# Optimization experiments

Hardware: AMD Instinct MI355X
Metric: run time of the kernel (lower is better)

The kernel has to match this reference:

```python
import jax, jax.numpy as jnp
import numpy as np

N = 100000
E = 3200000
F_IN = 256
F_OUT = 256
HID = 64


def setup_inputs() -> dict:
    key = jax.random.key(0)
    ks = jax.random.split(key, 16)
    stdv = 1.0 / np.sqrt(F_OUT)
    std_att = 1.0 / np.sqrt(HID)
    std_att_vec = 1.0 / np.sqrt(3.0)
    u = lambda k, shape, s: jax.random.uniform(k, shape, jnp.float32, -s, s)
    return {
        "inputx": jax.random.normal(ks[0], (N, F_IN), jnp.float32),
        "row_A": jax.random.randint(ks[1], (E,), 0, N),
        "col_A": jax.random.randint(ks[2], (E,), 0, N),
        "val_A": jax.random.uniform(ks[3], (E,), jnp.float32),
        "row_A2": jax.random.randint(ks[4], (E,), 0, N),
        "col_A2": jax.random.randint(ks[5], (E,), 0, N),
        "val_A2": jax.random.uniform(ks[6], (E,), jnp.float32),
        "weight_A": u(ks[7], (F_IN, F_OUT), stdv),
        "weight_A2": u(ks[8], (F_IN, F_OUT), stdv),
        "weight_mlp": u(ks[9], (F_IN, F_OUT), stdv),
        "W_k0": u(ks[10], (F_OUT, HID), std_att),
        "W_k1": u(ks[11], (F_OUT, HID), std_att),
        "W_k2": u(ks[12], (F_OUT, HID), std_att),
        "att_vec_A": u(ks[13], (F_OUT, HID), std_att),
        "att_vec_A2": u(ks[14], (F_OUT, HID), std_att),
        "att_vec_mlp": u(ks[15], (F_OUT, HID), std_att),
        "att_vec": u(jax.random.fold_in(key, 99), (3, 3), std_att_vec),
    }


def _spmm(row, col, val, x, n):
    # COO sparse-dense matmul: out[r] += val_e * x[c]
    return jax.ops.segment_sum(val[:, None] * x[col], row, num_segments=n)


def reference(inputx, row_A, col_A, val_A, row_A2, col_A2, val_A2,
              weight_A, weight_A2, weight_mlp, W_k0, W_k1, W_k2,
              att_vec_A, att_vec_A2, att_vec_mlp, att_vec):
    n = inputx.shape[0]
    out_A = jax.nn.relu(_spmm(row_A, col_A, val_A, inputx @ weight_A, n))
    out_A2 = jax.nn.relu(_spmm(row_A2, col_A2, val_A2, inputx @ weight_A2, n))
    out_mlp = jax.nn.relu(inputx @ weight_mlp)
    # attention gating
    T = 3.0
    k0 = jnp.mean(out_A @ W_k0, axis=0, keepdims=True)    # [1, HID]
    k1 = jnp.mean(out_A2 @ W_k1, axis=0, keepdims=True)
    k2 = jnp.mean(out_mlp @ W_k2, axis=0, keepdims=True)
    logits = jnp.concatenate([
        (out_A @ att_vec_A) @ k0.T,      # [N, 1]
        (out_A2 @ att_vec_A2) @ k1.T,
        (out_mlp @ att_vec_mlp) @ k2.T,
    ], axis=1)                           # [N, 3]
    att = jax.nn.softmax((jax.nn.sigmoid(logits) @ att_vec) / T, axis=1)
    return 3.0 * (att[:, 0:1] * out_A + att[:, 1:2] * out_A2 + att[:, 2:3] * out_mlp)
```

## Files before the change

kernel.cpp:

```cpp
#include <hip/hip_runtime.h>

typedef __bf16 bf16;
typedef __bf16 bf16x4 __attribute__((ext_vector_type(4)));
typedef __bf16 bf16x8 __attribute__((ext_vector_type(8)));
typedef float f32x4 __attribute__((ext_vector_type(4)));

__device__ __forceinline__ f32x4 bf2f(bf16x4 v){
  f32x4 r; r[0]=(float)v[0]; r[1]=(float)v[1]; r[2]=(float)v[2]; r[3]=(float)v[3]; return r;
}

#define NBMAX 1600
#define NBP   1601
#define CHUNK 16384

__global__ __launch_bounds__(256) void k_xcvt(const float* __restrict__ X, bf16* __restrict__ Xb, int total){
  int i = (blockIdx.x*256 + threadIdx.x)*8;
  if (i + 8 <= total){
    float4 a = *(const float4*)(X+i);
    float4 b = *(const float4*)(X+i+4);
    bf16x8 v;
    v[0]=(bf16)a.x; v[1]=(bf16)a.y; v[2]=(bf16)a.z; v[3]=(bf16)a.w;
    v[4]=(bf16)b.x; v[5]=(bf16)b.y; v[6]=(bf16)b.z; v[7]=(bf16)b.w;
    *(bf16x8*)(Xb+i) = v;
  }
}

__global__ __launch_bounds__(256) void k_wt(const float* __restrict__ W0, const float* __restrict__ W1,
                                            const float* __restrict__ W2, bf16* __restrict__ WT3){
  int n = blockIdx.x, mat = blockIdx.y, k = threadIdx.x;
  const float* W = (mat==0)?W0:((mat==1)?W1:W2);
  WT3[mat*65536 + n*256 + k] = (bf16)W[k*256 + n];
}

__global__ __launch_bounds__(512) void k_gemm(const bf16* __restrict__ Xb, const bf16* __restrict__ WT3,
        bf16* __restrict__ O0, bf16* __restrict__ O1, bf16* __restrict__ O2,
        float* __restrict__ colsum, int N){
  __shared__ __align__(16) bf16 sA[128*32];
  __shared__ __align__(16) bf16 sB[256*32];
  __shared__ float gcs[256];
  int t = threadIdx.x;
  int lane = t & 63, wave = t>>6, wm = wave>>2, wn = wave&3;
  int mat = blockIdx.x;
  int m0 = blockIdx.y*128;
  const bf16* WT = WT3 + mat*65536;
  bf16* OUT = (mat==0)?O0:((mat==1)?O1:O2);

  f32x4 acc[4][4];
#pragma unroll
  for (int i=0;i<4;i++)
#pragma unroll
    for (int j=0;j<4;j++){ acc[i][j][0]=0.f; acc[i][j][1]=0.f; acc[i][j][2]=0.f; acc[i][j][3]=0.f; }

  int ar = t>>2, ac = t&3;
  int alc = ac ^ ((ar>>1)&3);
  int agrow = m0 + ar; if (agrow > N-1) agrow = N-1;
  const bf16* gA = Xb + (size_t)agrow*256 + alc*8;
  bf16* lA = sA + ar*32 + ac*8;

  int br = t>>2, bc = t&3;
  int blc = bc ^ ((br>>1)&3);
  const bf16* gB0 = WT + br*256 + blc*8;
  const bf16* gB1 = WT + (br+128)*256 + blc*8;
  bf16* lB0 = sB + br*32 + bc*8;
  bf16* lB1 = sB + (br+128)*32 + bc*8;

  for (int k0=0; k0<256; k0+=32){
    __syncthreads();
    *(bf16x8*)lA  = *(const bf16x8*)(gA  + k0);
    *(bf16x8*)lB0 = *(const bf16x8*)(gB0 + k0);
    *(bf16x8*)lB1 = *(const bf16x8*)(gB1 + k0);
    __syncthreads();

    bf16x8 af[4], bfr[4];
#pragma unroll
    for (int i=0;i<4;i++){
      int arow = wm*64 + i*16 + (lane&15);
      int pc = (lane>>4) ^ ((arow>>1)&3);
      af[i] = *(const bf16x8*)(sA + arow*32 + pc*8);
    }
#pragma unroll
    for (int j=0;j<4;j++){
      int brow = wn*64 + j*16 + (lane&15);
      int pc = (lane>>4) ^ ((brow>>1)&3);
      bfr[j] = *(const bf16x8*)(sB + brow*32 + pc*8);
    }
#pragma unroll
    for (int i=0;i<4;i++)
#pragma unroll
      for (int j=0;j<4;j++)
        acc[i][j] = __builtin_amdgcn_mfma_f32_16x16x32_bf16(af[i], bfr[j], acc[i][j], 0,0,0);
  }

  int col0 = wn*64 + (lane&15);
  int rb = m0 + wm*64 + ((lane>>4)<<2);
  bool isrelu = (mat==2);
  float pj[4] = {0.f,0.f,0.f,0.f};
#pragma unroll
  for (int i=0;i<4;i++){
#pragma unroll
    for (int tt=0; tt<4; tt++){
      int r = rb + i*16 + tt;
      if (r < N){
#pragma unroll
        for (int j=0;j<4;j++){
          float vv = acc[i][j][tt];
          if (isrelu && vv < 0.f) vv = 0.f;
          if (isrelu) pj[j] += vv;
          OUT[(size_t)r*256 + col0 + j*16] = (bf16)vv;
        }
      }
    }
  }
  if (isrelu){
    if (t < 256) gcs[t] = 0.f;
    __syncthreads();
#pragma unroll
    for (int j=0;j<4;j++) atomicAdd(&gcs[col0 + j*16], pj[j]);
    __syncthreads();
    if (t < 256) atomicAdd(&colsum[512 + t], gcs[t]);
  }
}

__global__ __launch_bounds__(512) void k_bcnt(const int* __restrict__ rowA, const int* __restrict__ rowA2,
    int* __restrict__ bcnt, int* __restrict__ chist, int E, int NB){
  __shared__ int hist[NBMAX];
  int mat = blockIdx.y;
  const int* row = mat? rowA2 : rowA;
  int t = threadIdx.x;
  for (int i=t; i<NB; i+=512) hist[i] = 0;
  __syncthreads();
  int base = blockIdx.x * CHUNK;
  int endi = base + CHUNK; if (endi > E) endi = E;
  for (int i = base + t; i < endi; i += 512) atomicAdd(&hist[row[i] >> 6], 1);
  __syncthreads();
  int* ch = chist + ((size_t)(mat*gridDim.x + blockIdx.x))*NBMAX;
  for (int i=t; i<NB; i+=512){
    int c = hist[i];
    ch[i] = c;
    if (c) atomicAdd(&bcnt[mat*NBMAX + i], c);
  }
}

__global__ __launch_bounds__(256) void k_bscan(const int* __restrict__ bcnt, int* __restrict__ gstart,
    int* __restrict__ gcur, int NB, int E){
  __shared__ int ss[256];
  __shared__ int carry;
  int mat = blockIdx.x;
  int t = threadIdx.x;
  if (t==0) carry = 0;
  __syncthreads();
  for (int base=0; base<NB; base+=256){
    int i = base + t;
    int v = (i < NB) ? bcnt[mat*NBMAX + i] : 0;
    ss[t] = v; __syncthreads();
    for (int off=1; off<256; off<<=1){
      int u = (t>=off)? ss[t-off] : 0;
      __syncthreads();
      ss[t] += u;
      __syncthreads();
    }
    int excl = carry + ss[t] - v;
    if (i < NB){ gstart[mat*NBP + i] = excl; gcur[mat*NB + i] = excl; }
    int tot = ss[255];
    __syncthreads();
    if (t==0) carry += tot;
    __syncthreads();
  }
  if (t==0) gstart[mat*NBP + NB] = E;
}

__global__ __launch_bounds__(512) void k_binT(const int* __restrict__ rowA, const int* __restrict__ colA,
    const float* __restrict__ valA, const int* __restrict__ rowA2, const int* __restrict__ colA2,
    const float* __restrict__ valA2, int* __restrict__ gcur, const int* __restrict__ chist,
    int2* __restrict__ pTA, int2* __restrict__ pTA2, int E, int NB){
  __shared__ int hist[NBMAX];
  int mat = blockIdx.y;
  const int* row = mat? rowA2 : rowA;
  const int* col = mat? colA2 : colA;
  const float* val = mat? valA2 : valA;
  int2* pT = mat? pTA2 : pTA;
  int t = threadIdx.x;
  const int* ch = chist + ((size_t)(mat*gridDim.x + blockIdx.x))*NBMAX;
  for (int i=t; i<NB; i+=512) hist[i] = ch[i];
  __syncthreads();
  for (int i=t; i<NB; i+=512){
    int c = hist[i];
    if (c) hist[i] = atomicAdd(&gcur[mat*NB + i], c);
  }
  __syncthreads();
  int base = blockIdx.x * CHUNK;
  int endi = base + CHUNK; if (endi > E) endi = E;
  for (int i = base + t; i < endi; i += 512){
    int r = row[i];
    int pos = atomicAdd(&hist[r >> 6], 1);
    int2 p; p.x = ((r & 63) << 17) | col[i]; p.y = __float_as_int(val[i]);
    pT[pos] = p;
  }
}

__global__ __launch_bounds__(256) void k_csr(const int2* __restrict__ pTA, const int2* __restrict__ pTA2,
    const int* __restrict__ gstart, int* __restrict__ rsA, int* __restrict__ rsA2,
    int2* __restrict__ permA, int2* __restrict__ permA2, int N, int NB, int E){
  __shared__ int rowst[64];
  __shared__ int fill[64];
  int mat = blockIdx.y;
  const int2* pT = mat? pTA2 : pTA;
  int2* perm = mat? permA2 : permA;
  int* rs = mat? rsA2 : rsA;
  int b = blockIdx.x;
  int t = threadIdx.x;
  int r0 = b*64;
  int start = gstart[mat*NBP + b];
  int end   = gstart[mat*NBP + b + 1];
  if (t < 64) fill[t] = 0;
  __syncthreads();
  for (int i = start + t; i < end; i += 256) atomicAdd(&fill[pT[i].x >> 17], 1);
  __syncthreads();
  if (t < 64){
    int v = fill[t];
    int x = v;
#pragma unroll
    for (int off=1; off<64; off<<=1){
      int u = __shfl_up(x, off, 64);
      if (t >= off) x += u;
    }
    int st = start + x - v;
    rowst[t] = st;
    if (r0 + t < N) rs[r0 + t] = st;
    fill[t] = 0;
  }
  __syncthreads();
  for (int i = start + t; i < end; i += 256){
    int2 e = pT[i];
    int rl = e.x >> 17;
    int pos = atomicAdd(&fill[rl], 1);
    int2 o; o.x = e.x & 0x1FFFF; o.y = e.y;
    perm[rowst[rl] + pos] = o;
  }
  if (t == 0 && b == NB-1) rs[N] = E;
}

__global__ __launch_bounds__(256) void k_spmm(const bf16* __restrict__ XA, const bf16* __restrict__ XA2,
    const int* __restrict__ rsA, const int* __restrict__ rsA2,
    const int2* __restrict__ permA, const int2* __restrict__ permA2,
    bf16* __restrict__ outA, bf16* __restrict__ outA2, float* __restrict__ part, int N){
  __shared__ float scs[1024];
  int mat = blockIdx.y;
  const bf16* src = mat? XA2 : XA;
  const int* rs = mat? rsA2 : rsA;
  const int2* perm = mat? permA2 : permA;
  bf16* dst = mat? outA2 : outA;
  int t = threadIdx.x, lane = t & 63, wv = t >> 6;
  int c = lane*4;
  int rstep = gridDim.x*4;
  f32x4 csum; csum[0]=0.f; csum[1]=0.f; csum[2]=0.f; csum[3]=0.f;

  for (int row = blockIdx.x*4 + wv; row < N; row += rstep){
    int e = rs[row], eend = rs[row+1];
    f32x4 acc; acc[0]=0.f; acc[1]=0.f; acc[2]=0.f; acc[3]=0.f;

    int2 p0, p1, p2, p3;
    bool have = (e + 3 < eend);
    if (have){ p0 = perm[e]; p1 = perm[e+1]; p2 = perm[e+2]; p3 = perm[e+3]; }
    while (have){
      bf16x4 g0 = *(const bf16x4*)(src + (size_t)p0.x*256 + c);
      bf16x4 g1 = *(const bf16x4*)(src + (size_t)p1.x*256 + c);
      bf16x4 g2 = *(const bf16x4*)(src + (size_t)p2.x*256 + c);
      bf16x4 g3 = *(const bf16x4*)(src + (size_t)p3.x*256 + c);
      float v0 = __int_as_float(p0.y), v1 = __int_as_float(p1.y);
      float v2 = __int_as_float(p2.y), v3 = __int_as_float(p3.y);
      e += 4;
      have = (e + 3 < eend);
      if (have){ p0 = perm[e]; p1 = perm[e+1]; p2 = perm[e+2]; p3 = perm[e+3]; }
      acc += v0 * bf2f(g0);
      acc += v1 * bf2f(g1);
      acc += v2 * bf2f(g2);
      acc += v3 * bf2f(g3);
    }
    for (; e < eend; ++e){
      int2 p = perm[e];
      acc += __int_as_float(p.y) * bf2f(*(const bf16x4*)(src + (size_t)p.x*256 + c));
    }
    bf16x4 o;
#pragma unroll
    for (int k=0;k<4;k++){
      float v = acc[k] < 0.f ? 0.f : acc[k];
      o[k] = (bf16)v;
      csum[k] += v;
    }
    *(bf16x4*)(dst + (size_t)row*256 + c) = o;
  }

#pragma unroll
  for (int k=0;k<4;k++) scs[wv*256 + c + k] = csum[k];
  __syncthreads();
  if (wv == 0){
    float* pp = part + ((blockIdx.x & 7)*2 + mat)*256;
#pragma unroll
    for (int k=0;k<4;k++){
      float s = scs[c+k] + scs[256+c+k] + scs[512+c+k] + scs[768+c+k];
      atomicAdd(&pp[c+k], s);
    }
  }
}

__global__ void k_attn(const float* __restrict__ colsum, const float* __restrict__ part,
    const float* __restrict__ Wk0, const float* __restrict__ Wk1, const float* __restrict__ Wk2,
    const float* __restrict__ V0, const float* __restrict__ V1, const float* __restrict__ V2,
    float* __restrict__ wvec, int N){
  __shared__ float smean[768];
  __shared__ float sk[192];
  int t = threadIdx.x;
  float invN = 1.f/(float)N;
  float s0 = 0.f, s1 = 0.f;
#pragma unroll
  for (int s=0; s<8; s++){
    s0 += part[(s*2+0)*256 + t];
    s1 += part[(s*2+1)*256 + t];
  }
  smean[t]     = s0 * invN;
  smean[t+256] = s1 * invN;
  smean[t+512] = colsum[512+t] * invN;
  __syncthreads();
  if (t < 192){
    int j = t>>6, h = t&63;
    const float* Wk = (j==0)?Wk0:((j==1)?Wk1:Wk2);
    float s = 0.f;
    for (int cc=0; cc<256; cc++) s += smean[j*256+cc]*Wk[cc*64+h];
    sk[j*64+h] = s;
  }
  __syncthreads();
  int c = t;
  for (int j=0;j<3;j++){
    const float* V = (j==0)?V0:((j==1)?V1:V2);
    float s = 0.f;
    for (int h=0;h<64;h++) s += V[c*64+h]*sk[j*64+h];
    wvec[j*256+c] = s;
  }
}

__global__ __launch_bounds__(256) void k_epi(const bf16* __restrict__ A, const bf16* __restrict__ B,
    const bf16* __restrict__ M, const float* __restrict__ wvec, const float* __restrict__ av9,
    float* __restrict__ out, int N){
  __shared__ float sw[768];
  __shared__ float sav[9];
  int t = threadIdx.x;
  sw[t] = wvec[t]; sw[t+256] = wvec[t+256]; sw[t+512] = wvec[t+512];
  if (t < 9) sav[t] = av9[t];
  __syncthreads();
  int row = blockIdx.x*4 + (t>>6);
  if (row >= N) return;
  int lane = t & 63;
  int c = lane*4;
  f32x4 a = bf2f(*(const bf16x4*)(A + (size_t)row*256 + c));
  f32x4 b = bf2f(*(const bf16x4*)(B + (size_t)row*256 + c));
  f32x4 m = bf2f(*(const bf16x4*)(M + (size_t)row*256 + c));
  float p0 = a[0]*sw[c] + a[1]*sw[c+1] + a[2]*sw[c+2] + a[3]*sw[c+3];
  float p1 = b[0]*sw[256+c] + b[1]*sw[256+c+1] + b[2]*sw[256+c+2] + b[3]*sw[256+c+3];
  float p2 = m[0]*sw[512+c] + m[1]*sw[512+c+1] + m[2]*sw[512+c+2] + m[3]*sw[512+c+3];
#pragma unroll
  for (int off=32; off>=1; off>>=1){
    p0 += __shfl_xor(p0, off);
    p1 += __shfl_xor(p1, off);
    p2 += __shfl_xor(p2, off);
  }
  float s0 = 1.f/(1.f+expf(-p0));
  float s1 = 1.f/(1.f+expf(-p1));
  float s2 = 1.f/(1.f+expf(-p2));
  float g0 = (s0*sav[0] + s1*sav[3] + s2*sav[6]) * (1.f/3.f);
  float g1 = (s0*sav[1] + s1*sav[4] + s2*sav[7]) * (1.f/3.f);
  float g2 = (s0*sav[2] + s1*sav[5] + s2*sav[8]) * (1.f/3.f);
  float mx = fmaxf(g0, fmaxf(g1,g2));
  float e0 = expf(g0-mx), e1 = expf(g1-mx), e2 = expf(g2-mx);
  float inv = 3.f/(e0+e1+e2);
  float a0 = e0*inv, a1 = e1*inv, a2 = e2*inv;
  f32x4 o = a0*a + a1*b + a2*m;
  *(f32x4*)(out + (size_t)row*256 + c) = o;
}

extern "C" void kernel_launch(void* const* d_in, const int* in_sizes, int n_in,
                              void* d_out, int out_size, void* d_ws, size_t ws_size,
                              hipStream_t stream){
  const float* X    = (const float*)d_in[0];
  const int*   rowA = (const int*)d_in[1];
  const int*   colA = (const int*)d_in[2];
  const float* valA = (const float*)d_in[3];
  const int*   rowA2= (const int*)d_in[4];
  const int*   colA2= (const int*)d_in[5];
  const float* valA2= (const float*)d_in[6];
  const float* W0   = (const float*)d_in[7];
  const float* W1   = (const float*)d_in[8];
  const float* W2   = (const float*)d_in[9];
  const float* Wk0  = (const float*)d_in[10];
  const float* Wk1  = (const float*)d_in[11];
  const float* Wk2  = (const float*)d_in[12];
  const float* V0   = (const float*)d_in[13];
  const float* V1   = (const float*)d_in[14];
  const float* V2   = (const float*)d_in[15];
  const float* AV9  = (const float*)d_in[16];
  int N = in_sizes[0] / 256;
  int E = in_sizes[1];
  int NB = (N + 63) >> 6;
  int ebl2 = (E + CHUNK-1)/CHUNK;

  char* ws = (char*)d_ws;
  size_t off = 0;
  auto take = [&](size_t b)->char*{ char* r = ws + off; off = (off + b + 255) & ~(size_t)255; return r; };
  size_t mb = (size_t)N*256*2;
  bf16* WT3    = (bf16*)take((size_t)3*256*256*2);
  bf16* XbOutA = (bf16*)take(mb);
  bf16* XAb    = (bf16*)take(mb);
  bf16* XA2b   = (bf16*)take(mb);
  bf16* XMb    = (bf16*)take(mb);
  bf16* outA2b = (bf16*)take(mb);
  int* rsA    = (int*)take((size_t)(N+1)*4);
  int* rsA2   = (int*)take((size_t)(N+1)*4);
  int* gcur   = (int*)take((size_t)2*NB*4);
  int* bcnt   = (int*)take((size_t)2*NBMAX*4);
  int* gstart = (int*)take((size_t)2*NBP*4);
  int* chist  = (int*)take((size_t)2*ebl2*NBMAX*4);
  float* colsum = (float*)take(768*4);
  float* part   = (float*)take((size_t)8*2*256*4);
  float* wvec   = (float*)take(768*4);
  int2* permA  = (int2*)take((size_t)E*8);
  int2* permA2 = (int2*)take((size_t)E*8);
  int2* pTA  = (int2*)XbOutA;
  int2* pTA2 = pTA + E;

  hipMemsetAsync(bcnt, 0, (size_t)2*NBMAX*4, stream);
  hipMemsetAsync(colsum, 0, 768*4, stream);
  hipMemsetAsync(part, 0, (size_t)8*2*256*4, stream);

  int total = N*256;
  k_xcvt<<<dim3((total/8 + 255)/256),256,0,stream>>>(X, XbOutA, total);
  k_wt<<<dim3(256,3),256,0,stream>>>(W0,W1,W2,WT3);
  k_gemm<<<dim3(3,(N+127)/128),512,0,stream>>>(XbOutA, WT3, XAb, XA2b, XMb, colsum, N);
  k_bcnt<<<dim3(ebl2,2),512,0,stream>>>(rowA,rowA2,bcnt,chist,E,NB);
  k_bscan<<<2,256,0,stream>>>(bcnt,gstart,gcur,NB,E);
  k_binT<<<dim3(ebl2,2),512,0,stream>>>(rowA,colA,valA,rowA2,colA2,valA2,gcur,chist,pTA,pTA2,E,NB);
  k_csr<<<dim3(NB,2),256,0,stream>>>(pTA,pTA2,gstart,rsA,rsA2,permA,permA2,N,NB,E);
  int sblk = (N+31)/32;
  k_spmm<<<dim3(sblk,2),256,0,stream>>>(XAb,XA2b,rsA,rsA2,permA,permA2,XbOutA,outA2b,part,N);
  k_attn<<<1,256,0,stream>>>(colsum,part,Wk0,Wk1,Wk2,V0,V1,V2,wvec,N);
  k_epi<<<dim3((N+3)/4),256,0,stream>>>(XbOutA,outA2b,XMb,wvec,AV9,(float*)d_out,N);
}
```

Baseline: 1.057 ms.

## Reassociate to (A·X)·W: run SpMM on bf16 X, then fused in-place GEMM+ReLU

Applies matrix associativity so both sparse aggregations gather from the single bf16 copy of X, and the dense GEMM runs afterwards. The GEMM now applies ReLU and accumulates per-column sums for all three branches in place on the SpMM outputs and on X. This drops the per-block partial-sum scratch and its reduction, and cuts the workspace from five activation buffers to three. Both SpMM instances now share one gather source, which should improve cache reuse. The cost is an extra bf16 rounding of A·X before the GEMM, which changes numerics slightly.

```diff
diff --git a/kernel.cpp b/kernel.cpp
--- a/kernel.cpp
+++ b/kernel.cpp
@@ -30,95 +30,6 @@
   int n = blockIdx.x, mat = blockIdx.y, k = threadIdx.x;
   const float* W = (mat==0)?W0:((mat==1)?W1:W2);
   WT3[mat*65536 + n*256 + k] = (bf16)W[k*256 + n];
-}
-
-__global__ __launch_bounds__(512) void k_gemm(const bf16* __restrict__ Xb, const bf16* __restrict__ WT3,
-        bf16* __restrict__ O0, bf16* __restrict__ O1, bf16* __restrict__ O2,
-        float* __restrict__ colsum, int N){
-  __shared__ __align__(16) bf16 sA[128*32];
-  __shared__ __align__(16) bf16 sB[256*32];
-  __shared__ float gcs[256];
-  int t = threadIdx.x;
-  int lane = t & 63, wave = t>>6, wm = wave>>2, wn = wave&3;
-  int mat = blockIdx.x;
-  int m0 = blockIdx.y*128;
-  const bf16* WT = WT3 + mat*65536;
-  bf16* OUT = (mat==0)?O0:((mat==1)?O1:O2);
-
-  f32x4 acc[4][4];
-#pragma unroll
-  for (int i=0;i<4;i++)
-#pragma unroll
-    for (int j=0;j<4;j++){ acc[i][j][0]=0.f; acc[i][j][1]=0.f; acc[i][j][2]=0.f; acc[i][j][3]=0.f; }
-
-  int ar = t>>2, ac = t&3;
-  int alc = ac ^ ((ar>>1)&3);
-  int agrow = m0 + ar; if (agrow > N-1) agrow = N-1;
-  const bf16* gA = Xb + (size_t)agrow*256 + alc*8;
-  bf16* lA = sA + ar*32 + ac*8;
-
-  int br = t>>2, bc = t&3;
-  int blc = bc ^ ((br>>1)&3);
-  const bf16* gB0 = WT + br*256 + blc*8;
-  const bf16* gB1 = WT + (br+128)*256 + blc*8;
-  bf16* lB0 = sB + br*32 + bc*8;
-  bf16* lB1 = sB + (br+128)*32 + bc*8;
-
-  for (int k0=0; k0<256; k0+=32){
-    __syncthreads();
-    *(bf16x8*)lA  = *(const bf16x8*)(gA  + k0);
-    *(bf16x8*)lB0 = *(const bf16x8*)(gB0 + k0);
-    *(bf16x8*)lB1 = *(const bf16x8*)(gB1 + k0);
-    __syncthreads();
-
-    bf16x8 af[4], bfr[4];
-#pragma unroll
-    for (int i=0;i<4;i++){
-      int arow = wm*64 + i*16 + (lane&15);
-      int pc = (lane>>4) ^ ((arow>>1)&3);
-      af[i] = *(const bf16x8*)(sA + arow*32 + pc*8);
-    }
-#pragma unroll
-    for (int j=0;j<4;j++){
-      int brow = wn*64 + j*16 + (lane&15);
-      int pc = (lane>>4) ^ ((brow>>1)&3);
-      bfr[j] = *(const bf16x8*)(sB + brow*32 + pc*8);
-    }
-#pragma unroll
-    for (int i=0;i<4;i++)
-#pragma unroll
-      for (int j=0;j<4;j++)
-        acc[i][j] = __builtin_amdgcn_mfma_f32_16x16x32_bf16(af[i], bfr[j], acc[i][j], 0,0,0);
-  }
-
-  int col0 = wn*64 + (lane&15);
-  int rb = m0 + wm*64 + ((lane>>4)<<2);
-  bool isrelu = (mat==2);
-  float pj[4] = {0.f,0.f,0.f,0.f};
-#pragma unroll
-  for (int i=0;i<4;i++){
-#pragma unroll
-    for (int tt=0; tt<4; tt++){
-      int r = rb + i*16 + tt;
-      if (r < N){
-#pragma unroll
-        for (int j=0;j<4;j++){
-          float vv = acc[i][j][tt];
-          if (isrelu && vv < 0.f) vv = 0.f;
-          if (isrelu) pj[j] += vv;
-          OUT[(size_t)r*256 + col0 + j*16] = (bf16)vv;
-        }
-      }
-    }
-  }
-  if (isrelu){
-    if (t < 256) gcs[t] = 0.f;
-    __syncthreads();
-#pragma unroll
-    for (int j=0;j<4;j++) atomicAdd(&gcs[col0 + j*16], pj[j]);
-    __syncthreads();
-    if (t < 256) atomicAdd(&colsum[512 + t], gcs[t]);
-  }
 }
 
 __global__ __launch_bounds__(512) void k_bcnt(const int* __restrict__ rowA, const int* __restrict__ rowA2,
@@ -240,20 +151,17 @@
   if (t == 0 && b == NB-1) rs[N] = E;
 }
 
-__global__ __launch_bounds__(256) void k_spmm(const bf16* __restrict__ XA, const bf16* __restrict__ XA2,
+__global__ __launch_bounds__(256) void k_spmm(const bf16* __restrict__ Xb,
     const int* __restrict__ rsA, const int* __restrict__ rsA2,
     const int2* __restrict__ permA, const int2* __restrict__ permA2,
-    bf16* __restrict__ outA, bf16* __restrict__ outA2, float* __restrict__ part, int N){
-  __shared__ float scs[1024];
+    bf16* __restrict__ AXb, bf16* __restrict__ A2Xb, int N){
   int mat = blockIdx.y;
-  const bf16* src = mat? XA2 : XA;
   const int* rs = mat? rsA2 : rsA;
   const int2* perm = mat? permA2 : permA;
-  bf16* dst = mat? outA2 : outA;
+  bf16* dst = mat? A2Xb : AXb;
   int t = threadIdx.x, lane = t & 63, wv = t >> 6;
   int c = lane*4;
   int rstep = gridDim.x*4;
-  f32x4 csum; csum[0]=0.f; csum[1]=0.f; csum[2]=0.f; csum[3]=0.f;
 
   for (int row = blockIdx.x*4 + wv; row < N; row += rstep){
     int e = rs[row], eend = rs[row+1];
@@ -263,10 +171,10 @@
     bool have = (e + 3 < eend);
     if (have){ p0 = perm[e]; p1 = perm[e+1]; p2 = perm[e+2]; p3 = perm[e+3]; }
     while (have){
-      bf16x4 g0 = *(const bf16x4*)(src + (size_t)p0.x*256 + c);
-      bf16x4 g1 = *(const bf16x4*)(src + (size_t)p1.x*256 + c);
-      bf16x4 g2 = *(const bf16x4*)(src + (size_t)p2.x*256 + c);
-      bf16x4 g3 = *(const bf16x4*)(src + (size_t)p3.x*256 + c);
+      bf16x4 g0 = *(const bf16x4*)(Xb + (size_t)p0.x*256 + c);
+      bf16x4 g1 = *(const bf16x4*)(Xb + (size_t)p1.x*256 + c);
+      bf16x4 g2 = *(const bf16x4*)(Xb + (size_t)p2.x*256 + c);
+      bf16x4 g3 = *(const bf16x4*)(Xb + (size_t)p3.x*256 + c);
       float v0 = __int_as_float(p0.y), v1 = __int_as_float(p1.y);
       float v2 = __int_as_float(p2.y), v3 = __int_as_float(p3.y);
       e += 4;
@@ -279,32 +187,101 @@
     }
     for (; e < eend; ++e){
       int2 p = perm[e];
-      acc += __int_as_float(p.y) * bf2f(*(const bf16x4*)(src + (size_t)p.x*256 + c));
+      acc += __int_as_float(p.y) * bf2f(*(const bf16x4*)(Xb + (size_t)p.x*256 + c));
     }
     bf16x4 o;
 #pragma unroll
-    for (int k=0;k<4;k++){
-      float v = acc[k] < 0.f ? 0.f : acc[k];
-      o[k] = (bf16)v;
-      csum[k] += v;
-    }
+    for (int k=0;k<4;k++) o[k] = (bf16)acc[k];
     *(bf16x4*)(dst + (size_t)row*256 + c) = o;
   }
-
-#pragma unroll
-  for (int k=0;k<4;k++) scs[wv*256 + c + k] = csum[k];
-  __syncthreads();
-  if (wv == 0){
-    float* pp = part + ((blockIdx.x & 7)*2 + mat)*256;
-#pragma unroll
-    for (int k=0;k<4;k++){
-      float s = scs[c+k] + scs[256+c+k] + scs[512+c+k] + scs[768+c+k];
-      atomicAdd(&pp[c+k], s);
-    }
-  }
-}
-
-__global__ void k_attn(const float* __restrict__ colsum, const float* __restrict__ part,
+}
+
+__global__ __launch_bounds__(512) void k_gemm(bf16* __restrict__ M0, bf16* __restrict__ M1,
+        bf16* __restrict__ M2, const bf16* __restrict__ WT3, float* __restrict__ colsum, int N){
+  __shared__ __align__(16) bf16 sA[128*32];
+  __shared__ __align__(16) bf16 sB[256*32];
+  __shared__ float gcs[256];
+  int t = threadIdx.x;
+  int lane = t & 63, wave = t>>6, wm = wave>>2, wn = wave&3;
+  int mat = blockIdx.y;
+  int m0 = blockIdx.x*128;
+  const bf16* WT = WT3 + mat*65536;
+  bf16* M = (mat==0)?M0:((mat==1)?M1:M2);
+
+  f32x4 acc[4][4];
+#pragma unroll
+  for (int i=0;i<4;i++)
+#pragma unroll
+    for (int j=0;j<4;j++){ acc[i][j][0]=0.f; acc[i][j][1]=0.f; acc[i][j][2]=0.f; acc[i][j][3]=0.f; }
+
+  int ar = t>>2, ac = t&3;
+  int alc = ac ^ ((ar>>1)&3);
+  int agrow = m0 + ar; if (agrow > N-1) agrow = N-1;
+  const bf16* gA = M + (size_t)agrow*256 + alc*8;
+  bf16* lA = sA + ar*32 + ac*8;
+
+  int br = t>>2, bc = t&3;
+  int blc = bc ^ ((br>>1)&3);
+  const bf16* gB0 = WT + br*256 + blc*8;
+  const bf16* gB1 = WT + (br+128)*256 + blc*8;
+  bf16* lB0 = sB + br*32 + bc*8;
+  bf16* lB1 = sB + (br+128)*32 + bc*8;
+
+  for (int k0=0; k0<256; k0+=32){
+    __syncthreads();
+    *(bf16x8*)lA  = *(const bf16x8*)(gA  + k0);
+    *(bf16x8*)lB0 = *(const bf16x8*)(gB0 + k0);
+    *(bf16x8*)lB1 = *(const bf16x8*)(gB1 + k0);
+    __syncthreads();
+
+    bf16x8 af[4], bfr[4];
+#pragma unroll
+    for (int i=0;i<4;i++){
+      int arow = wm*64 + i*16 + (lane&15);
+      int pc = (lane>>4) ^ ((arow>>1)&3);
+      af[i] = *(const bf16x8*)(sA + arow*32 + pc*8);
+    }
+#pragma unroll
+    for (int j=0;j<4;j++){
+      int brow = wn*64 + j*16 + (lane&15);
+      int pc = (lane>>4) ^ ((brow>>1)&3);
+      bfr[j] = *(const bf16x8*)(sB + brow*32 + pc*8);
+    }
+#pragma unroll
+    for (int i=0;i<4;i++)
+#pragma unroll
+      for (int j=0;j<4;j++)
+        acc[i][j] = __builtin_amdgcn_mfma_f32_16x16x32_bf16(af[i], bfr[j], acc[i][j], 0,0,0);
+  }
+
+  int col0 = wn*64 + (lane&15);
+  int rb = m0 + wm*64 + ((lane>>4)<<2);
+  float pj[4] = {0.f,0.f,0.f,0.f};
+#pragma unroll
+  for (int i=0;i<4;i++){
+#pragma unroll
+    for (int tt=0; tt<4; tt++){
+      int r = rb + i*16 + tt;
+      if (r < N){
+#pragma unroll
+        for (int j=0;j<4;j++){
+          float vv = acc[i][j][tt];
+          if (vv < 0.f) vv = 0.f;
+          pj[j] += vv;
+          M[(size_t)r*256 + col0 + j*16] = (bf16)vv;
+        }
+      }
+    }
+  }
+  if (t < 256) gcs[t] = 0.f;
+  __syncthreads();
+#pragma unroll
+  for (int j=0;j<4;j++) atomicAdd(&gcs[col0 + j*16], pj[j]);
+  __syncthreads();
+  if (t < 256) atomicAdd(&colsum[mat*256 + t], gcs[t]);
+}
+
+__global__ void k_attn(const float* __restrict__ colsum,
     const float* __restrict__ Wk0, const float* __restrict__ Wk1, const float* __restrict__ Wk2,
     const float* __restrict__ V0, const float* __restrict__ V1, const float* __restrict__ V2,
     float* __restrict__ wvec, int N){
@@ -312,15 +289,9 @@
   __shared__ float sk[192];
   int t = threadIdx.x;
   float invN = 1.f/(float)N;
-  float s0 = 0.f, s1 = 0.f;
-#pragma unroll
-  for (int s=0; s<8; s++){
-    s0 += part[(s*2+0)*256 + t];
-    s1 += part[(s*2+1)*256 + t];
-  }
-  smean[t]     = s0 * invN;
-  smean[t+256] = s1 * invN;
-  smean[t+512] = colsum[512+t] * invN;
+  smean[t]     = colsum[t]     * invN;
+  smean[t+256] = colsum[t+256] * invN;
+  smean[t+512] = colsum[t+512] * invN;
   __syncthreads();
   if (t < 192){
     int j = t>>6, h = t&63;
@@ -407,12 +378,10 @@
   size_t off = 0;
   auto take = [&](size_t b)->char*{ char* r = ws + off; off = (off + b + 255) & ~(size_t)255; return r; };
   size_t mb = (size_t)N*256*2;
-  bf16* WT3    = (bf16*)take((size_t)3*256*256*2);
-  bf16* XbOutA = (bf16*)take(mb);
-  bf16* XAb    = (bf16*)take(mb);
-  bf16* XA2b   = (bf16*)take(mb);
-  bf16* XMb    = (bf16*)take(mb);
-  bf16* outA2b = (bf16*)take(mb);
+  bf16* WT3  = (bf16*)take((size_t)3*256*256*2);
+  bf16* Xb   = (bf16*)take(mb);
+  bf16* B1   = (bf16*)take(mb);
+  bf16* B2   = (bf16*)take(mb);
   int* rsA    = (int*)take((size_t)(N+1)*4);
   int* rsA2   = (int*)take((size_t)(N+1)*4);
   int* gcur   = (int*)take((size_t)2*NB*4);
@@ -420,27 +389,25 @@
   int* gstart = (int*)take((size_t)2*NBP*4);
   int* chist  = (int*)take((size_t)2*ebl2*NBMAX*4);
   float* colsum = (float*)take(768*4);
-  float* part   = (float*)take((size_t)8*2*256*4);
   float* wvec   = (float*)take(768*4);
   int2* permA  = (int2*)take((size_t)E*8);
   int2* permA2 = (int2*)take((size_t)E*8);
-  int2* pTA  = (int2*)XbOutA;
-  int2* pTA2 = pTA + E;
+  int2* pTA  = (int2*)B1;
+  int2* pTA2 = (int2*)B2;
 
   hipMemsetAsync(bcnt, 0, (size_t)2*NBMAX*4, stream);
   hipMemsetAsync(colsum, 0, 768*4, stream);
-  hipMemsetAsync(part, 0, (size_t)8*2*256*4, stream);
 
   int total = N*256;
-  k_xcvt<<<dim3((total/8 + 255)/256),256,0,stream>>>(X, XbOutA, total);
+  k_xcvt<<<dim3((total/8 + 255)/256),256,0,stream>>>(X, Xb, total);
   k_wt<<<dim3(256,3),256,0,stream>>>(W0,W1,W2,WT3);
-  k_gemm<<<dim3(3,(N+127)/128),512,0,stream>>>(XbOutA, WT3, XAb, XA2b, XMb, colsum, N);
   k_bcnt<<<dim3(ebl2,2),512,0,stream>>>(rowA,rowA2,bcnt,chist,E,NB);
   k_bscan<<<2,256,0,stream>>>(bcnt,gstart,gcur,NB,E);
   k_binT<<<dim3(ebl2,2),512,0,stream>>>(rowA,colA,valA,rowA2,colA2,valA2,gcur,chist,pTA,pTA2,E,NB);
   k_csr<<<dim3(NB,2),256,0,stream>>>(pTA,pTA2,gstart,rsA,rsA2,permA,permA2,N,NB,E);
   int sblk = (N+31)/32;
-  k_spmm<<<dim3(sblk,2),256,0,stream>>>(XAb,XA2b,rsA,rsA2,permA,permA2,XbOutA,outA2b,part,N);
-  k_attn<<<1,256,0,stream>>>(colsum,part,Wk0,Wk1,Wk2,V0,V1,V2,wvec,N);
-  k_epi<<<dim3((N+3)/4),256,0,stream>>>(XbOutA,outA2b,XMb,wvec,AV9,(float*)d_out,N);
-}
+  k_spmm<<<dim3(sblk,2),256,0,stream>>>(Xb,rsA,rsA2,permA,permA2,B1,B2,N);
+  k_gemm<<<dim3((N+127)/128,3),512,0,stream>>>(B1,B2,Xb,WT3,colsum,N);
+  k_attn<<<1,256,0,stream>>>(colsum,Wk0,Wk1,Wk2,V0,V1,V2,wvec,N);
+  k_epi<<<dim3((N+3)/4),256,0,stream>>>(B1,B2,Xb,wvec,AV9,(float*)d_out,N);
+}
```

New measurement: 1.067 ms. Within noise of the previous version (+0.9%).
